# Kernel optimization log

Measured on AMD Instinct MI355X. Metric: run time of the kernel, lower is better.

The kernel has to match this reference:

```python
import jax, jax.numpy as jnp
import numpy as np

B, T, D, N = 16, 4096, 512, 3


def _window_sum(x, k):
    # x: [B, T, ...] -> sliding-window sum of size k, stride 1 -> [B, T-k+1, ...]
    c = jnp.cumsum(x, axis=1)
    c = jnp.concatenate([jnp.zeros_like(c[:, :1]), c], axis=1)
    return c[:, k:] - c[:, :-k]


def setup_inputs() -> dict:
    key = jax.random.key(0)
    ks = jax.random.split(key, 7)
    s_prev = jax.random.normal(ks[0], (B, D), jnp.float32)
    enc_hs = jax.random.normal(ks[1], (B, T, D), jnp.float32)
    # realistic padding mask: True = padded position
    lengths = jax.random.randint(ks[2], (B,), T // 2, T + 1)
    src_mask = jnp.arange(T)[None, :] >= lengths[:, None]
    scale = 1.0 / np.sqrt(D)
    Vw = jax.random.normal(ks[3], (N, D, D), jnp.float32) * scale
    Vb = jax.random.normal(ks[4], (N, D), jnp.float32) * 0.01
    Ww = jax.random.normal(ks[5], (N, D, D), jnp.float32) * scale
    Wb = jax.random.normal(ks[6], (N, D), jnp.float32) * 0.01
    return {"s_prev": s_prev, "enc_hs": enc_hs, "src_mask": src_mask,
            "Vw": Vw, "Vb": Vb, "Ww": Ww, "Wb": Wb}


def _level(s_prev, hs, mask, vw, vb, ww, wb):
    # hs: [B, L, D], mask: [B, L] (True = masked)
    # torch Linear: y = x @ W^T + b, weight is [out, in]
    v = jnp.einsum('bld,ed->ble', hs, vw) + vb            # V_i(hs)
    att = jnp.einsum('bd,bld->bl', s_prev, v)             # bmm(s_prev, V(hs)^T)
    att = jnp.where(mask, -jnp.inf, att)
    att = jax.nn.softmax(att, axis=-1)                    # [B, L]
    pooled = jnp.einsum('bl,bld->bd', att, hs)            # bmm(att, hs)
    ctx = pooled @ ww.T + wb                              # W_i(.)
    return ctx, att


def reference(s_prev, enc_hs, src_mask, Vw, Vb, Ww, Wb):
    ctx, att = _level(s_prev, enc_hs, src_mask, Vw[0], Vb[0], Ww[0], Wb[0])
    for i in range(1, N):
        k = i + 1
        hs_ngram = _window_sum(enc_hs, k) / k                      # AvgPool1d(k,1)
        n_mask = _window_sum(src_mask.astype(jnp.float32), k) > 0  # any masked in window
        c, _ = _level(s_prev, hs_ngram, n_mask, Vw[i], Vb[i], Ww[i], Wb[i])
        ctx = ctx + c
    return ctx, att
```

## Files before the change

### kernel.cpp

```cpp
#include <hip/hip_runtime.h>

#define BB 16
#define TT 4096
#define DD 512
#define CH 16
#define NY (TT/CH)
#define NEG (-1.0e30f)

#define OFF_Q     64
#define OFF_QP    (OFF_Q + 3*BB*DD)
#define OFF_P0    (OFF_QP + 4*3*BB*DD)
#define OFF_M     (OFF_P0 + BB*TT)
#define OFF_S     (OFF_M + 3*BB*NY)
#define OFF_SC    (OFF_S + 3*BB*NY)
#define OFF_MT    (OFF_SC + 3*BB*NY)
#define OFF_TOT   (OFF_MT + 64)
#define OFF_PART  (OFF_TOT + 64)
#define OFF_POOL  (OFF_PART + 3*NY*BB*DD)

__global__ void __launch_bounds__(1024) k_lengths(const unsigned char* mask, int* lengths) {
    __shared__ int sflag;
    const int tid = threadIdx.x;
    if (tid == 0) sflag = 0;
    __syncthreads();
    int f = 0;
    for (int idx = tid * 4 + 1; idx < BB * TT; idx += 1024 * 4)
        f |= (mask[idx] != 0);
    if (f) atomicOr(&sflag, 1);
    __syncthreads();
    const bool byte_layout = (sflag != 0);
    const int* m32 = (const int*)mask;
    const int b = tid >> 6;
    const int lane = tid & 63;
    int cnt = 0;
    if (byte_layout) {
        for (int t = lane; t < TT; t += 64) cnt += (mask[b * TT + t] != 0);
    } else {
        for (int t = lane; t < TT; t += 64) cnt += (m32[b * TT + t] != 0);
    }
    #pragma unroll
    for (int m = 32; m >= 1; m >>= 1) cnt += __shfl_xor(cnt, m, 64);
    if (lane == 0) lengths[b] = TT - cnt;
}

__global__ void __launch_bounds__(256) k_q(const float* __restrict__ s_prev,
                                           const float* __restrict__ Vw,
                                           float* __restrict__ qpart) {
    const int blk = blockIdx.x;
    const int ec = blk & 3;
    const int ib = blk >> 2;
    const int b = ib % BB;
    const int i = ib / BB;
    const int d0 = threadIdx.x;
    const float* sp = s_prev + b * DD + ec * 128;
    const float* W = Vw + (size_t)i * DD * DD + (size_t)(ec * 128) * DD;
    float a0 = 0.f, a1 = 0.f;
    for (int e = 0; e < 128; e++) {
        const float se = sp[e];
        a0 += se * W[e * DD + d0];
        a1 += se * W[e * DD + d0 + 256];
    }
    qpart[(size_t)blk * DD + d0] = a0;
    qpart[(size_t)blk * DD + d0 + 256] = a1;
}

__global__ void __launch_bounds__(256) k_q_reduce(const float* __restrict__ qpart,
                                                  float* __restrict__ q) {
    const int idx = blockIdx.x * 256 + threadIdx.x;
    const int ib = idx / DD;
    const int d = idx % DD;
    float s = 0.f;
    #pragma unroll
    for (int ec = 0; ec < 4; ec++) s += qpart[(size_t)(ib * 4 + ec) * DD + d];
    q[idx] = s;
}

__global__ void __launch_bounds__(256) k_fused(const float* __restrict__ enc,
                                               const float* __restrict__ q,
                                               const int* __restrict__ lengths,
                                               float* __restrict__ p0,
                                               float* __restrict__ mbuf,
                                               float* __restrict__ sbuf,
                                               float* __restrict__ part) {
    __shared__ float sp[CH + 2][3];
    __shared__ float svs[3][CH];
    __shared__ float su[3][CH];
    __shared__ float sm[3];
    const int b = blockIdx.x;
    const int y = blockIdx.y;
    const int t0 = y * CH;
    const int len = lengths[b];
    const int tid = threadIdx.x;
    if (t0 >= len) {
        if (tid < 3) {
            mbuf[(size_t)(tid * BB + b) * NY + y] = NEG;
            sbuf[(size_t)(tid * BB + b) * NY + y] = 0.f;
        }
        return;
    }
    const int wv = tid >> 6, lane = tid & 63;

    const float4* q40 = (const float4*)(q + (size_t)(0 * BB + b) * DD);
    const float4* q41 = (const float4*)(q + (size_t)(1 * BB + b) * DD);
    const float4* q42 = (const float4*)(q + (size_t)(2 * BB + b) * DD);
    const float4 qa0 = q40[lane], qb0 = q40[64 + lane];
    const float4 qa1 = q41[lane], qb1 = q41[64 + lane];
    const float4 qa2 = q42[lane], qb2 = q42[64 + lane];
    #pragma unroll
    for (int rr = 0; rr < 5; rr++) {
        if (rr == 4 && wv >= 2) break;
        const int r = (rr < 4) ? (wv + rr * 4) : (CH + wv);
        const int t = t0 + r;
        float d0 = 0.f, d1 = 0.f, d2 = 0.f;
        if (t < len) {
            const float4* e4 = (const float4*)(enc + ((size_t)b * TT + t) * DD);
            const float4 x0 = e4[lane], x1 = e4[64 + lane];
            d0 = x0.x*qa0.x + x0.y*qa0.y + x0.z*qa0.z + x0.w*qa0.w
               + x1.x*qb0.x + x1.y*qb0.y + x1.z*qb0.z + x1.w*qb0.w;
            d1 = x0.x*qa1.x + x0.y*qa1.y + x0.z*qa1.z + x0.w*qa1.w
               + x1.x*qb1.x + x1.y*qb1.y + x1.z*qb1.z + x1.w*qb1.w;
            d2 = x0.x*qa2.x + x0.y*qa2.y + x0.z*qa2.z + x0.w*qa2.w
               + x1.x*qb2.x + x1.y*qb2.y + x1.z*qb2.z + x1.w*qb2.w;
            #pragma unroll
            for (int m = 32; m >= 1; m >>= 1) {
                d0 += __shfl_xor(d0, m, 64);
                d1 += __shfl_xor(d1, m, 64);
                d2 += __shfl_xor(d2, m, 64);
            }
        }
        if (lane == 0) {
            sp[r][0] = d0; sp[r][1] = d1; sp[r][2] = d2;
            if (rr < 4 && t < len) p0[(size_t)b * TT + t] = d0;
        }
    }
    __syncthreads();

    if (tid < 48) {
        const int i = tid / CH, r = tid % CH;
        const int l = t0 + r;
        const bool valid = l < (len - i);
        float s = sp[r][i];
        if (i > 0) s += sp[r + 1][i];
        if (i > 1) s += sp[r + 2][i];
        svs[i][r] = valid ? s * (1.0f / (float)(i + 1)) : NEG;
    }
    __syncthreads();
    if (tid < 3) {
        float m = NEG;
        #pragma unroll
        for (int r = 0; r < CH; r++) m = fmaxf(m, svs[tid][r]);
        sm[tid] = m;
    }
    __syncthreads();
    if (tid < 48) {
        const int i = tid / CH, r = tid % CH;
        const bool valid = (t0 + r) < (len - i);
        su[i][r] = valid ? __expf(svs[i][r] - sm[i]) : 0.f;
    }
    __syncthreads();
    if (tid < 3) {
        float s = 0.f;
        #pragma unroll
        for (int r = 0; r < CH; r++) s += su[tid][r];
        mbuf[(size_t)(tid * BB + b) * NY + y] = sm[tid];
        sbuf[(size_t)(tid * BB + b) * NY + y] = s;
    }
    __syncthreads();

    const int d = tid * 2;
    const float* col = enc + (size_t)b * TT * DD + d;
    float2 va, vb2, vc;
    {
        const int t = t0;
        va  = (t     < TT) ? *(const float2*)(col + (size_t)t * DD)       : make_float2(0.f, 0.f);
        vb2 = (t + 1 < TT) ? *(const float2*)(col + (size_t)(t + 1) * DD) : make_float2(0.f, 0.f);
    }
    float2 a0 = {0, 0}, a1 = {0, 0}, a2 = {0, 0};
    #pragma unroll
    for (int r = 0; r < CH; r++) {
        const int t = t0 + r;
        vc = (t + 2 < TT) ? *(const float2*)(col + (size_t)(t + 2) * DD) : make_float2(0.f, 0.f);
        const float u0 = su[0][r], u1 = su[1][r], u2 = su[2][r];
        const float w1x = va.x + vb2.x, w1y = va.y + vb2.y;
        const float w2x = w1x + vc.x,   w2y = w1y + vc.y;
        a0.x += u0 * va.x;  a0.y += u0 * va.y;
        a1.x += u1 * w1x;   a1.y += u1 * w1y;
        a2.x += u2 * w2x;   a2.y += u2 * w2y;
        va = vb2; vb2 = vc;
    }
    a1.x *= 0.5f; a1.y *= 0.5f;
    a2.x *= (1.0f / 3.0f); a2.y *= (1.0f / 3.0f);
    float* pt = part + (size_t)y * BB * DD + (size_t)b * DD + d;
    *(float2*)(pt)                        = a0;
    *(float2*)(pt + (size_t)NY * BB * DD)     = a1;
    *(float2*)(pt + (size_t)2 * NY * BB * DD) = a2;
}

__global__ void __launch_bounds__(256) k_combine(const float* __restrict__ mbuf,
                                                 const float* __restrict__ sbuf,
                                                 float* __restrict__ scale,
                                                 float* __restrict__ mtot,
                                                 float* __restrict__ tot) {
    const int g = blockIdx.x * 4 + (threadIdx.x >> 6);
    const int lane = threadIdx.x & 63;
    const float* mv = mbuf + (size_t)g * NY;
    const float* sv = sbuf + (size_t)g * NY;
    float ml[4], sl[4];
    float m = NEG;
    #pragma unroll
    for (int j = 0; j < 4; j++) {
        ml[j] = mv[lane * 4 + j];
        sl[j] = sv[lane * 4 + j];
        m = fmaxf(m, ml[j]);
    }
    #pragma unroll
    for (int s = 32; s >= 1; s >>= 1) m = fmaxf(m, __shfl_xor(m, s, 64));
    float t = 0.f;
    #pragma unroll
    for (int j = 0; j < 4; j++) t += sl[j] * __expf(ml[j] - m);
    #pragma unroll
    for (int s = 32; s >= 1; s >>= 1) t += __shfl_xor(t, s, 64);
    const float inv = 1.0f / t;
    #pragma unroll
    for (int j = 0; j < 4; j++)
        scale[(size_t)g * NY + lane * 4 + j] = __expf(ml[j] - m) * inv;
    if (lane == 0) { mtot[g] = m; tot[g] = t; }
}

__global__ void __launch_bounds__(256) k_reduce(const float* __restrict__ part,
                                                const float* __restrict__ scale,
                                                float* __restrict__ pooled) {
    const int idx = blockIdx.x * 256 + threadIdx.x;
    const int ib = idx / DD;
    const int d = idx % DD;
    const int i = ib / BB, b = ib % BB;
    const float* sc = scale + (size_t)ib * NY;
    const float* base = part + (size_t)i * NY * BB * DD + (size_t)b * DD + d;
    float s = 0.f;
    #pragma unroll 8
    for (int y = 0; y < NY; y++) s += base[(size_t)y * BB * DD] * sc[y];
    pooled[idx] = s;
}

__global__ void __launch_bounds__(256) k_att(const float* __restrict__ p0,
                                             const int* __restrict__ lengths,
                                             const float* __restrict__ mtot,
                                             const float* __restrict__ tot,
                                             float* __restrict__ att) {
    const int idx = blockIdx.x * 256 + threadIdx.x;
    const int b = idx >> 12;
    const int t = idx & (TT - 1);
    const float m = mtot[b];
    const float inv = 1.0f / tot[b];
    att[idx] = (t < lengths[b]) ? __expf(p0[idx] - m) * inv : 0.f;
}

__global__ void __launch_bounds__(256) k_ctx(const float* __restrict__ pooled,
                                             const float* __restrict__ Ww,
                                             const float* __restrict__ Wb,
                                             float* __restrict__ ctx) {
    const int wid = blockIdx.x * 4 + (threadIdx.x >> 6);
    const int lane = threadIdx.x & 63;
    const int b = wid >> 9;
    const int e = wid & 511;
    float acc = 0.f;
    #pragma unroll
    for (int i = 0; i < 3; i++) {
        const float4* pr = (const float4*)(pooled + (size_t)(i * BB + b) * DD);
        const float4* wr = (const float4*)(Ww + ((size_t)i * DD + e) * DD);
        const float4 p0 = pr[lane], p1 = pr[64 + lane];
        const float4 w0 = wr[lane], w1 = wr[64 + lane];
        acc += p0.x * w0.x + p0.y * w0.y + p0.z * w0.z + p0.w * w0.w
             + p1.x * w1.x + p1.y * w1.y + p1.z * w1.z + p1.w * w1.w;
    }
    #pragma unroll
    for (int m = 32; m >= 1; m >>= 1) acc += __shfl_xor(acc, m, 64);
    if (lane == 0)
        ctx[(size_t)b * DD + e] = acc + Wb[e] + Wb[DD + e] + Wb[2 * DD + e];
}

extern "C" void kernel_launch(void* const* d_in, const int* in_sizes, int n_in,
                              void* d_out, int out_size, void* d_ws, size_t ws_size,
                              hipStream_t stream) {
    const float* s_prev = (const float*)d_in[0];
    const float* enc    = (const float*)d_in[1];
    const void*  mask   = d_in[2];
    const float* Vw     = (const float*)d_in[3];
    const float* Ww     = (const float*)d_in[5];
    const float* Wb     = (const float*)d_in[6];

    float* out = (float*)d_out;
    float* ctx = out;
    float* att = out + BB * DD;

    float* W       = (float*)d_ws;
    int*   lengths = (int*)d_ws;
    float* q       = W + OFF_Q;
    float* qpart   = W + OFF_QP;
    float* p0      = W + OFF_P0;
    float* mbuf    = W + OFF_M;
    float* sbuf    = W + OFF_S;
    float* scale   = W + OFF_SC;
    float* mtot    = W + OFF_MT;
    float* tot     = W + OFF_TOT;
    float* part    = W + OFF_PART;
    float* pooled  = W + OFF_POOL;

    k_lengths<<<1, 1024, 0, stream>>>((const unsigned char*)mask, lengths);
    k_q<<<192, 256, 0, stream>>>(s_prev, Vw, qpart);
    k_q_reduce<<<3 * BB * DD / 256, 256, 0, stream>>>(qpart, q);
    k_fused<<<dim3(BB, NY), 256, 0, stream>>>(enc, q, lengths, p0, mbuf, sbuf, part);
    k_combine<<<12, 256, 0, stream>>>(mbuf, sbuf, scale, mtot, tot);
    k_reduce<<<3 * BB * DD / 256, 256, 0, stream>>>(part, scale, pooled);
    k_att<<<BB * TT / 256, 256, 0, stream>>>(p0, lengths, mtot, tot, att);
    k_ctx<<<BB * DD / 4, 256, 0, stream>>>(pooled, Ww, Wb, ctx);
}
```

Measured before the change: 266.6 us.

## Double chunk size, fuse attention output into combine, parallelize length count

Raises the per-block time chunk from 16 to 32 rows. This halves the number of partial sums that k_reduce must read and the partial-buffer traffic, at the cost of fewer blocks in the fused kernel. The k_att kernel is removed: the level-0 attention probabilities are now written inside k_combine, which uses one block per (level, batch) group. k_lengths now runs one block per batch instead of a single block, which spreads the mask scan across more compute units.

New measurement: 275.5 us. +3.3%, slower.

```diff
diff --git a/kernel.cpp b/kernel.cpp
--- a/kernel.cpp
+++ b/kernel.cpp
@@ -3,7 +3,7 @@
 #define BB 16
 #define TT 4096
 #define DD 512
-#define CH 16
+#define CH 32
 #define NY (TT/CH)
 #define NEG (-1.0e30f)
 
@@ -13,34 +13,35 @@
 #define OFF_M     (OFF_P0 + BB*TT)
 #define OFF_S     (OFF_M + 3*BB*NY)
 #define OFF_SC    (OFF_S + 3*BB*NY)
-#define OFF_MT    (OFF_SC + 3*BB*NY)
-#define OFF_TOT   (OFF_MT + 64)
-#define OFF_PART  (OFF_TOT + 64)
+#define OFF_PART  (OFF_SC + 3*BB*NY)
 #define OFF_POOL  (OFF_PART + 3*NY*BB*DD)
 
-__global__ void __launch_bounds__(1024) k_lengths(const unsigned char* mask, int* lengths) {
+__global__ void __launch_bounds__(256) k_lengths(const unsigned char* mask, int* lengths) {
     __shared__ int sflag;
+    __shared__ int sred[4];
     const int tid = threadIdx.x;
+    const int b = blockIdx.x;
     if (tid == 0) sflag = 0;
     __syncthreads();
     int f = 0;
-    for (int idx = tid * 4 + 1; idx < BB * TT; idx += 1024 * 4)
+    for (int idx = tid * 4 + 1; idx < BB * TT; idx += 256 * 4)
         f |= (mask[idx] != 0);
     if (f) atomicOr(&sflag, 1);
     __syncthreads();
     const bool byte_layout = (sflag != 0);
     const int* m32 = (const int*)mask;
-    const int b = tid >> 6;
-    const int lane = tid & 63;
     int cnt = 0;
     if (byte_layout) {
-        for (int t = lane; t < TT; t += 64) cnt += (mask[b * TT + t] != 0);
+        for (int t = tid; t < TT; t += 256) cnt += (mask[b * TT + t] != 0);
     } else {
-        for (int t = lane; t < TT; t += 64) cnt += (m32[b * TT + t] != 0);
+        for (int t = tid; t < TT; t += 256) cnt += (m32[b * TT + t] != 0);
     }
     #pragma unroll
     for (int m = 32; m >= 1; m >>= 1) cnt += __shfl_xor(cnt, m, 64);
-    if (lane == 0) lengths[b] = TT - cnt;
+    if ((tid & 63) == 0) sred[tid >> 6] = cnt;
+    __syncthreads();
+    if (tid == 0)
+        lengths[b] = TT - (sred[0] + sred[1] + sred[2] + sred[3]);
 }
 
 __global__ void __launch_bounds__(256) k_q(const float* __restrict__ s_prev,
@@ -107,9 +108,9 @@
     const float4 qa1 = q41[lane], qb1 = q41[64 + lane];
     const float4 qa2 = q42[lane], qb2 = q42[64 + lane];
     #pragma unroll
-    for (int rr = 0; rr < 5; rr++) {
-        if (rr == 4 && wv >= 2) break;
-        const int r = (rr < 4) ? (wv + rr * 4) : (CH + wv);
+    for (int rr = 0; rr < CH / 4 + 1; rr++) {
+        if (rr == CH / 4 && wv >= 2) break;
+        const int r = (rr < CH / 4) ? (wv + rr * 4) : (CH + wv);
         const int t = t0 + r;
         float d0 = 0.f, d1 = 0.f, d2 = 0.f;
         if (t < len) {
@@ -130,12 +131,12 @@
         }
         if (lane == 0) {
             sp[r][0] = d0; sp[r][1] = d1; sp[r][2] = d2;
-            if (rr < 4 && t < len) p0[(size_t)b * TT + t] = d0;
+            if (rr < CH / 4 && t < len) p0[(size_t)b * TT + t] = d0;
         }
     }
     __syncthreads();
 
-    if (tid < 48) {
+    if (tid < 3 * CH) {
         const int i = tid / CH, r = tid % CH;
         const int l = t0 + r;
         const bool valid = l < (len - i);
@@ -152,7 +153,7 @@
         sm[tid] = m;
     }
     __syncthreads();
-    if (tid < 48) {
+    if (tid < 3 * CH) {
         const int i = tid / CH, r = tid % CH;
         const bool valid = (t0 + r) < (len - i);
         su[i][r] = valid ? __expf(svs[i][r] - sm[i]) : 0.f;
@@ -191,40 +192,49 @@
     a1.x *= 0.5f; a1.y *= 0.5f;
     a2.x *= (1.0f / 3.0f); a2.y *= (1.0f / 3.0f);
     float* pt = part + (size_t)y * BB * DD + (size_t)b * DD + d;
-    *(float2*)(pt)                        = a0;
+    *(float2*)(pt)                            = a0;
     *(float2*)(pt + (size_t)NY * BB * DD)     = a1;
     *(float2*)(pt + (size_t)2 * NY * BB * DD) = a2;
 }
 
 __global__ void __launch_bounds__(256) k_combine(const float* __restrict__ mbuf,
                                                  const float* __restrict__ sbuf,
+                                                 const float* __restrict__ p0,
+                                                 const int* __restrict__ lengths,
                                                  float* __restrict__ scale,
-                                                 float* __restrict__ mtot,
-                                                 float* __restrict__ tot) {
-    const int g = blockIdx.x * 4 + (threadIdx.x >> 6);
-    const int lane = threadIdx.x & 63;
-    const float* mv = mbuf + (size_t)g * NY;
-    const float* sv = sbuf + (size_t)g * NY;
-    float ml[4], sl[4];
-    float m = NEG;
-    #pragma unroll
-    for (int j = 0; j < 4; j++) {
-        ml[j] = mv[lane * 4 + j];
-        sl[j] = sv[lane * 4 + j];
-        m = fmaxf(m, ml[j]);
-    }
-    #pragma unroll
-    for (int s = 32; s >= 1; s >>= 1) m = fmaxf(m, __shfl_xor(m, s, 64));
-    float t = 0.f;
-    #pragma unroll
-    for (int j = 0; j < 4; j++) t += sl[j] * __expf(ml[j] - m);
-    #pragma unroll
-    for (int s = 32; s >= 1; s >>= 1) t += __shfl_xor(t, s, 64);
-    const float inv = 1.0f / t;
-    #pragma unroll
-    for (int j = 0; j < 4; j++)
-        scale[(size_t)g * NY + lane * 4 + j] = __expf(ml[j] - m) * inv;
-    if (lane == 0) { mtot[g] = m; tot[g] = t; }
+                                                 float* __restrict__ att) {
+    __shared__ float sred[4];
+    __shared__ float sbc;
+    const int g = blockIdx.x;
+    const int i = g / BB, b = g % BB;
+    const int tid = threadIdx.x;
+    const float ml = (tid < NY) ? mbuf[(size_t)g * NY + tid] : NEG;
+    const float sl = (tid < NY) ? sbuf[(size_t)g * NY + tid] : 0.f;
+    float v = ml;
+    #pragma unroll
+    for (int m = 32; m >= 1; m >>= 1) v = fmaxf(v, __shfl_xor(v, m, 64));
+    if ((tid & 63) == 0) sred[tid >> 6] = v;
+    __syncthreads();
+    if (tid == 0) sbc = fmaxf(fmaxf(sred[0], sred[1]), fmaxf(sred[2], sred[3]));
+    __syncthreads();
+    const float gm = sbc;
+    __syncthreads();
+    const float e = (tid < NY) ? __expf(ml - gm) : 0.f;
+    v = sl * e;
+    #pragma unroll
+    for (int m = 32; m >= 1; m >>= 1) v += __shfl_xor(v, m, 64);
+    if ((tid & 63) == 0) sred[tid >> 6] = v;
+    __syncthreads();
+    if (tid == 0) sbc = sred[0] + sred[1] + sred[2] + sred[3];
+    __syncthreads();
+    const float inv = 1.0f / sbc;
+    if (tid < NY) scale[(size_t)g * NY + tid] = e * inv;
+    if (i == 0) {
+        const int len = lengths[b];
+        for (int t = tid; t < TT; t += 256)
+            att[(size_t)b * TT + t] =
+                (t < len) ? __expf(p0[(size_t)b * TT + t] - gm) * inv : 0.f;
+    }
 }
 
 __global__ void __launch_bounds__(256) k_reduce(const float* __restrict__ part,
@@ -242,19 +252,6 @@
     pooled[idx] = s;
 }
 
-__global__ void __launch_bounds__(256) k_att(const float* __restrict__ p0,
-                                             const int* __restrict__ lengths,
-                                             const float* __restrict__ mtot,
-                                             const float* __restrict__ tot,
-                                             float* __restrict__ att) {
-    const int idx = blockIdx.x * 256 + threadIdx.x;
-    const int b = idx >> 12;
-    const int t = idx & (TT - 1);
-    const float m = mtot[b];
-    const float inv = 1.0f / tot[b];
-    att[idx] = (t < lengths[b]) ? __expf(p0[idx] - m) * inv : 0.f;
-}
-
 __global__ void __launch_bounds__(256) k_ctx(const float* __restrict__ pooled,
                                              const float* __restrict__ Ww,
                                              const float* __restrict__ Wb,
@@ -301,17 +298,14 @@
     float* mbuf    = W + OFF_M;
     float* sbuf    = W + OFF_S;
     float* scale   = W + OFF_SC;
-    float* mtot    = W + OFF_MT;
-    float* tot     = W + OFF_TOT;
     float* part    = W + OFF_PART;
     float* pooled  = W + OFF_POOL;
 
-    k_lengths<<<1, 1024, 0, stream>>>((const unsigned char*)mask, lengths);
+    k_lengths<<<BB, 256, 0, stream>>>((const unsigned char*)mask, lengths);
     k_q<<<192, 256, 0, stream>>>(s_prev, Vw, qpart);
     k_q_reduce<<<3 * BB * DD / 256, 256, 0, stream>>>(qpart, q);
     k_fused<<<dim3(BB, NY), 256, 0, stream>>>(enc, q, lengths, p0, mbuf, sbuf, part);
-    k_combine<<<12, 256, 0, stream>>>(mbuf, sbuf, scale, mtot, tot);
+    k_combine<<<3 * BB, 256, 0, stream>>>(mbuf, sbuf, p0, lengths, scale, att);
     k_reduce<<<3 * BB * DD / 256, 256, 0, stream>>>(part, scale, pooled);
-    k_att<<<BB * TT / 256, 256, 0, stream>>>(p0, lengths, mtot, tot, att);
     k_ctx<<<BB * DD / 4, 256, 0, stream>>>(pooled, Ww, Wb, ctx);
 }
```
